# Performance work log

Measured on AMD Instinct MI355X. Metric: run time of the kernel, lower is better.

## Reference

```python
import jax, jax.numpy as jnp
import numpy as np
from jax import lax

B, S, D, V, MAXLEN = 32, 2048, 1024, 32000, 2048
EPS = jnp.finfo(jnp.float32).eps  # torch RMSNorm default eps=None -> finfo eps


def setup_inputs() -> dict:
    key = jax.random.key(0)
    ks = jax.random.split(key, 10)
    w = lambda k, shape: (jax.random.normal(k, shape, jnp.float32) * 0.02)
    return {
        "x": jax.random.randint(ks[0], (B, S), 0, V),
        "emb": w(ks[1], (V, D)),
        "pos": w(ks[2], (MAXLEN, D)),
        "conv_w": w(ks[3], (3, D, D)),            # HIO layout (k, in, out)
        "conv_b": jnp.zeros((D,), jnp.float32),
        "wg1": w(ks[4], (D, D)), "bg1": jnp.zeros((D,), jnp.float32),
        "wmv": w(ks[5], (2 * D, D)), "bmv": jnp.zeros((D,), jnp.float32),
        "wmg": w(ks[6], (2 * D, D)), "bmg": jnp.zeros((D,), jnp.float32),
        "wrg": w(ks[7], (2 * D, D)), "brg": jnp.zeros((D,), jnp.float32),
        "rms_w": jnp.ones((D,), jnp.float32),
        "wp": w(ks[8], (2 * D, V)), "bp": jnp.zeros((V,), jnp.float32),
    }


def _rmsnorm(v, rms_w):
    ms = jnp.mean(v * v, axis=-1, keepdims=True)
    return v * lax.rsqrt(ms + EPS) * rms_w


def reference(x, emb, pos, conv_w, conv_b, wg1, bg1, wmv, bmv, wmg, bmg,
              wrg, brg, rms_w, wp, bp):
    seq_len = x.shape[1]
    h = emb[x] + pos[:seq_len]                     # [B, S, D]
    # Conv1d(D, D, k=3, padding=1) over the sequence axis
    h = lax.conv_general_dilated(h, conv_w, window_strides=(1,),
                                 padding=((1, 1),),
                                 dimension_numbers=("NHC", "HIO", "NHC")) + conv_b
    nodes = h * jax.nn.sigmoid(h @ wg1 + bg1)      # gated nodes [B, S, D]

    curr = nodes[:, :-1, :]                        # nodes_past [B, S-1, D]
    while curr.shape[1] > 1:                       # log2(S) static levels
        if curr.shape[1] % 2 != 0:
            curr = jnp.concatenate([curr, curr[:, -1:, :]], axis=1)
        left = curr[:, 0::2, :]
        right = curr[:, 1::2, :]
        combined = jnp.concatenate([left, right], axis=-1)   # [B, n/2, 2D]
        val = combined @ wmv + bmv
        gate = jax.nn.sigmoid(combined @ wmg + bmg)
        merged = _rmsnorm(val * gate, rms_w)
        res_gate = jax.nn.sigmoid(combined @ wrg + brg)
        residual = (left + right) * 0.5
        curr = res_gate * merged + (1.0 - res_gate) * residual

    root = curr[:, 0, :]                           # [B, D]
    last = nodes[:, -2, :]                         # last of nodes_past
    context = jnp.concatenate([root, last], axis=-1)  # [B, 2D]
    return context @ wp + bp                       # logits [B, V]
```

## Files before the change

kernel.cpp:

```cpp
#include <hip/hip_runtime.h>
#include <stdint.h>

typedef __bf16 bf16_t;
typedef __attribute__((ext_vector_type(8))) __bf16 bf16x8;
typedef __attribute__((ext_vector_type(4))) __bf16 bf16x4;
typedef __attribute__((ext_vector_type(4))) float f32x4;

#define NB 32
#define NS 2048
#define ND 1024
#define NV 32000
#define SP 2050

__device__ __forceinline__ float sigmoid_(float x) { return 1.0f / (1.0f + __expf(-x)); }

__device__ __forceinline__ void gload_lds16(const void* g, void* lds) {
  __builtin_amdgcn_global_load_lds((const __attribute__((address_space(1))) void*)g,
                                   (__attribute__((address_space(3))) void*)lds, 16, 0, 0);
}


__global__ void zero_pad_k(bf16_t* h0p) {
  int i = blockIdx.x;
  int b = i >> 1;
  size_t row = (size_t)b * SP + ((i & 1) ? (SP - 1) : 0);
  bf16x4 z = {};
  *(bf16x4*)(h0p + row * ND + threadIdx.x * 4) = z;
}

__global__ void embed_k(const int* __restrict__ x, const float* __restrict__ emb,
                        const float* __restrict__ pos, bf16_t* __restrict__ h0p) {
  int bs = blockIdx.x;
  int b = bs >> 11, s = bs & (NS - 1);
  int idx = x[bs];
  const float* e = emb + (size_t)idx * ND;
  const float* p = pos + (size_t)s * ND;
  bf16_t* o = h0p + ((size_t)b * SP + s + 1) * ND;
  int d = threadIdx.x * 4;
  f32x4 ev = *(const f32x4*)(e + d);
  f32x4 pv = *(const f32x4*)(p + d);
  bf16x4 ov;
  ov[0] = (bf16_t)(ev[0] + pv[0]);
  ov[1] = (bf16_t)(ev[1] + pv[1]);
  ov[2] = (bf16_t)(ev[2] + pv[2]);
  ov[3] = (bf16_t)(ev[3] + pv[3]);
  *(bf16x4*)(o + d) = ov;
}

__global__ void conv_transpose_k(const float* __restrict__ in, bf16_t* __restrict__ out,
                                 int R, int C) {
  __shared__ float tile[32][33];
  int tc = blockIdx.x * 32, tr = blockIdx.y * 32;
  int tx = threadIdx.x;
  for (int i = threadIdx.y; i < 32; i += 8)
    tile[i][tx] = in[(size_t)(tr + i) * C + tc + tx];
  __syncthreads();
  for (int i = threadIdx.y; i < 32; i += 8)
    out[(size_t)(tc + i) * R + tr + tx] = (bf16_t)tile[tx][i];
}

__global__ void dup_row_k(bf16_t* nodes) {
  int b = blockIdx.x;
  const bf16_t* src = nodes + ((size_t)b * NS + NS - 2) * ND;
  bf16_t* dst = nodes + ((size_t)b * NS + NS - 1) * ND;
  int d = threadIdx.x * 4;
  *(bf16x4*)(dst + d) = *(const bf16x4*)(src + d);
}

__global__ void concat3_k(const float* __restrict__ a, const float* __restrict__ b,
                          const float* __restrict__ c, float* __restrict__ o) {
  int i = blockIdx.x * 256 + threadIdx.x;
  o[i] = i < 1024 ? a[i] : (i < 2048 ? b[i - 1024] : c[i - 2048]);
}

template <int EPI>
__global__ __launch_bounds__(512, 2) void gemm256(
    const bf16_t* __restrict__ A, const bf16_t* __restrict__ Bt,
    const float* __restrict__ bias, const void* aux, void* Cout,
    int M, int N, int K, int lda, int batchShift, int batchPad,
    int GX, int gpx, int nxg, int ych) {
  const int tid = threadIdx.x;
  const int lane = tid & 63;
  const int wave = tid >> 6;
  int n0, m0;
  if (nxg == 0) {
    n0 = (blockIdx.x % GX) * 256;
    m0 = (blockIdx.x / GX) * 256;
  } else {
    const int id = blockIdx.x;
    const int xcd = id & 7;
    const int jb = id >> 3;
    const int xg = xcd % nxg;
    const int ysub = xcd / nxg;
    n0 = (xg * gpx + (jb % gpx)) * 256;
    m0 = (ysub * ych + (jb / gpx)) * 256;
  }
  const int waveM = wave >> 2, waveN = wave & 3;

  __shared__ __align__(16) bf16_t sA[2][256 * 64];
  __shared__ __align__(16) bf16_t sB[2][256 * 64];

  const int srow = tid >> 3;
  const int sj = tid & 7;
  const bf16_t* pA[4];
  const bf16_t* pB[4];
#pragma unroll
  for (int idx = 0; idx < 4; ++idx) {
    int lr = idx * 64 + srow;
    int sc = sj ^ (lr & 7);
    int gm = m0 + lr;
    if (gm > M - 1) gm = M - 1;
    size_t grow = (size_t)gm + (size_t)(((unsigned)gm) >> batchShift) * batchPad;
    pA[idx] = A + grow * (size_t)lda + sc * 8;
    int gn = n0 + lr;
    if (gn > N - 1) gn = N - 1;
    pB[idx] = Bt + (size_t)gn * K + sc * 8;
  }
  const int ldsrow = wave * 8;

  auto stageA4 = [&](int buf) {
#pragma unroll
    for (int idx = 0; idx < 4; ++idx) {
      gload_lds16(pA[idx], &sA[buf][(size_t)(idx * 64 + ldsrow) * 64]);
      pA[idx] += 64;
    }
  };
  auto stageB4 = [&](int buf) {
#pragma unroll
    for (int idx = 0; idx < 4; ++idx) {
      gload_lds16(pB[idx], &sB[buf][(size_t)(idx * 64 + ldsrow) * 64]);
      pB[idx] += 64;
    }
  };

  const int rlane = lane & 15;
  const int klane = lane >> 4;
  int offA[8][2], offB[4][2];
#pragma unroll
  for (int i = 0; i < 8; ++i) {
    int ra = waveM * 128 + i * 16 + rlane;
#pragma unroll
    for (int ks = 0; ks < 2; ++ks)
      offA[i][ks] = ra * 128 + (((ks * 4 + klane) ^ (ra & 7)) << 4);
  }
#pragma unroll
  for (int j = 0; j < 4; ++j) {
    int rb = waveN * 64 + j * 16 + rlane;
#pragma unroll
    for (int ks = 0; ks < 2; ++ks)
      offB[j][ks] = rb * 128 + (((ks * 4 + klane) ^ (rb & 7)) << 4);
  }

  f32x4 acc[8][4] = {};

  const int nt = K >> 6;
  stageA4(0);
  stageB4(0);
  stageB4(1);
  asm volatile("s_waitcnt vmcnt(4)" ::: "memory");
  __builtin_amdgcn_s_barrier();

  for (int tt = 0; tt < nt; tt += 2) {
#pragma unroll
    for (int u = 0; u < 2; ++u) {
      const int t = tt + u;
      bf16x8 bfr[4][2];
#pragma unroll
      for (int j = 0; j < 4; ++j)
#pragma unroll
        for (int ks = 0; ks < 2; ++ks)
          bfr[j][ks] = *(const bf16x8*)((const char*)&sB[u][0] + offB[j][ks]);
      asm volatile("" ::: "memory");
      bf16x8 a0[4][2];
#pragma unroll
      for (int i = 0; i < 4; ++i)
#pragma unroll
        for (int ks = 0; ks < 2; ++ks)
          a0[i][ks] = *(const bf16x8*)((const char*)&sA[u][0] + offA[i][ks]);
      asm volatile("s_waitcnt lgkmcnt(8)" ::: "memory");
      __builtin_amdgcn_s_barrier();
      if (t + 1 < nt) stageA4(u ^ 1);
      if (t + 2 < nt) stageB4(u);
      __builtin_amdgcn_s_setprio(1);
#pragma unroll
      for (int ks = 0; ks < 2; ++ks)
#pragma unroll
        for (int i = 0; i < 4; ++i)
#pragma unroll
          for (int j = 0; j < 4; ++j)
            acc[i][j] = __builtin_amdgcn_mfma_f32_16x16x32_bf16(
                a0[i][ks], bfr[j][ks], acc[i][j], 0, 0, 0);
      __builtin_amdgcn_s_setprio(0);
      bf16x8 a1[4][2];
#pragma unroll
      for (int i = 0; i < 4; ++i)
#pragma unroll
        for (int ks = 0; ks < 2; ++ks)
          a1[i][ks] = *(const bf16x8*)((const char*)&sA[u][0] + offA[4 + i][ks]);
      __builtin_amdgcn_s_setprio(1);
#pragma unroll
      for (int ks = 0; ks < 2; ++ks)
#pragma unroll
        for (int i = 0; i < 4; ++i)
#pragma unroll
          for (int j = 0; j < 4; ++j)
            acc[4 + i][j] = __builtin_amdgcn_mfma_f32_16x16x32_bf16(
                a1[i][ks], bfr[j][ks], acc[4 + i][j], 0, 0, 0);
      __builtin_amdgcn_s_setprio(0);
      if (t + 2 < nt)
        asm volatile("s_waitcnt vmcnt(4)" ::: "memory");
      else
        asm volatile("s_waitcnt vmcnt(0)" ::: "memory");
      __builtin_amdgcn_s_barrier();
    }
  }

  const int colBase = n0 + waveN * 64 + rlane;
#pragma unroll
  for (int i = 0; i < 8; ++i) {
    const int rowBase = m0 + waveM * 128 + i * 16 + klane * 4;
#pragma unroll
    for (int j = 0; j < 4; ++j) {
      const int col = colBase + j * 16;
      const float bv = bias[col];
#pragma unroll
      for (int r = 0; r < 4; ++r) {
        const int row = rowBase + r;
        if (row >= M) continue;
        float v = acc[i][j][r] + bv;
        size_t o = (size_t)row * N + col;
        if constexpr (EPI == 0) {
          ((bf16_t*)Cout)[o] = (bf16_t)v;
        } else if constexpr (EPI == 1) {
          float hh = (float)((const bf16_t*)aux)[o];
          ((bf16_t*)Cout)[o] = (bf16_t)(hh * sigmoid_(v));
        } else {
          ((bf16_t*)Cout)[o] = (bf16_t)(col < 1024 ? v : sigmoid_(v));
        }
      }
    }
  }
}

template <bool ATOMIC>
__global__ __launch_bounds__(256, 2) void gemm128s(
    const bf16_t* __restrict__ A, const bf16_t* __restrict__ Bt,
    const float* __restrict__ bias, float* __restrict__ Cout,
    int M, int kLen, int nxy) {
  const int tid = threadIdx.x;
  const int lane = tid & 63;
  const int wave = tid >> 6;
  const int id = blockIdx.x;
  const int sk = id / nxy;
  const int rb2 = id % nxy;
  const int n0 = (rb2 % 24) * 128;
  const int m0 = (rb2 / 24) * 128;
  const int kOff = sk * kLen;

  const int waveM = wave >> 1, waveN = wave & 1;

  __shared__ __align__(16) bf16_t sA[2][128 * 64];
  __shared__ __align__(16) bf16_t sB[2][128 * 64];

  f32x4 acc[4][4] = {};

  const int srow = wave * 8 + (lane >> 3);
  const int sj = lane & 7;

  auto stage = [&](int buf, int kk0) {
#pragma unroll
    for (int j = 0; j < 4; ++j) {
      int rowT = j * 32 + srow;
      int k8 = sj ^ (rowT & 7);
      int gm = m0 + rowT;
      if (gm > M - 1) gm = M - 1;
      gload_lds16(A + (size_t)gm * 2048 + (kk0 + k8 * 8), &sA[buf][(j * 256 + wave * 64) * 8]);
      int gn = n0 + rowT;
      gload_lds16(Bt + (size_t)gn * 2048 + (kk0 + k8 * 8), &sB[buf][(j * 256 + wave * 64) * 8]);
    }
  };

  stage(0, kOff);
  __syncthreads();

  const int nt = kLen >> 6;
  int cur = 0;
  const int ar = waveM * 64 + (lane & 15);
  const int br = waveN * 64 + (lane & 15);
  const int kb0 = lane >> 4;

  for (int t = 0; t < nt; ++t) {
    if (t + 1 < nt) stage(cur ^ 1, kOff + (t + 1) * 64);

    const bf16_t* sa = sA[cur];
    const bf16_t* sb = sB[cur];
    bf16x8 af[2][4], bfr[2][4];
#pragma unroll
    for (int ks = 0; ks < 2; ++ks) {
      int kb = kb0 + ks * 4;
#pragma unroll
      for (int i = 0; i < 4; ++i) {
        int ra = ar + i * 16;
        af[ks][i] = *(const bf16x8*)&sa[ra * 64 + ((kb ^ (ra & 7)) * 8)];
        int rbq = br + i * 16;
        bfr[ks][i] = *(const bf16x8*)&sb[rbq * 64 + ((kb ^ (rbq & 7)) * 8)];
      }
    }
#pragma unroll
    for (int ks = 0; ks < 2; ++ks)
#pragma unroll
      for (int i = 0; i < 4; ++i)
#pragma unroll
        for (int j = 0; j < 4; ++j)
          acc[i][j] = __builtin_amdgcn_mfma_f32_16x16x32_bf16(af[ks][i], bfr[ks][j], acc[i][j], 0, 0, 0);
    __syncthreads();
    cur ^= 1;
  }

  const int colBase = n0 + waveN * 64 + (lane & 15);
#pragma unroll
  for (int i = 0; i < 4; ++i) {
    const int rowBase = m0 + waveM * 64 + i * 16 + (lane >> 4) * 4;
#pragma unroll
    for (int jj = 0; jj < 4; ++jj) {
      const int col = colBase + jj * 16;
      const float bv = (!ATOMIC || kOff == 0) ? bias[col] : 0.0f;
#pragma unroll
      for (int r = 0; r < 4; ++r) {
        const int row = rowBase + r;
        if (row >= M) continue;
        float v = acc[i][jj][r] + bv;
        size_t o = (size_t)row * 3072 + col;
        if constexpr (ATOMIC)
          atomicAdd(&Cout[o], v);
        else
          Cout[o] = v;
      }
    }
  }
}

__global__ __launch_bounds__(256) void tree_combine_k(
    const bf16_t* __restrict__ fb, const bf16_t* __restrict__ cur,
    const float* __restrict__ rms_w, bf16_t* __restrict__ outb) {
  const int m = blockIdx.x;
  const int t = threadIdx.x;
  const int d = t * 4;
  const bf16_t* row = fb + (size_t)m * 3072;
  bf16x4 vb = *(const bf16x4*)(row + d);
  bf16x4 gb = *(const bf16x4*)(row + 1024 + d);
  bf16x4 rb = *(const bf16x4*)(row + 2048 + d);
  f32x4 vg;
#pragma unroll
  for (int k = 0; k < 4; ++k) vg[k] = (float)vb[k] * (float)gb[k];
  float ss = vg[0] * vg[0] + vg[1] * vg[1] + vg[2] * vg[2] + vg[3] * vg[3];
#pragma unroll
  for (int o = 32; o > 0; o >>= 1) ss += __shfl_xor(ss, o);
  __shared__ float red[4];
  if ((t & 63) == 0) red[t >> 6] = ss;
  __syncthreads();
  float ms = (red[0] + red[1] + red[2] + red[3]) * (1.0f / ND);
  float scale = rsqrtf(ms + 1.1920929e-07f);
  f32x4 w = *(const f32x4*)(rms_w + d);
  const bf16_t* c0 = cur + (size_t)m * 2048;
  bf16x4 lv = *(const bf16x4*)(c0 + d);
  bf16x4 rv = *(const bf16x4*)(c0 + ND + d);
  bf16x4 o4;
#pragma unroll
  for (int k = 0; k < 4; ++k) {
    float merged = vg[k] * scale * w[k];
    float resid = 0.5f * ((float)lv[k] + (float)rv[k]);
    float g = (float)rb[k];
    o4[k] = (bf16_t)(g * merged + (1.0f - g) * resid);
  }
  *(bf16x4*)(outb + (size_t)m * ND + d) = o4;
}

__global__ __launch_bounds__(256) void tree_combine32_k(
    const float* __restrict__ fb, const bf16_t* __restrict__ cur,
    const float* __restrict__ rms_w, bf16_t* __restrict__ outb) {
  const int m = blockIdx.x;
  const int t = threadIdx.x;
  const int d = t * 4;
  const float* row = fb + (size_t)m * 3072;
  f32x4 v = *(const f32x4*)(row + d);
  f32x4 gl = *(const f32x4*)(row + 1024 + d);
  f32x4 rl = *(const f32x4*)(row + 2048 + d);
  f32x4 vg;
#pragma unroll
  for (int k = 0; k < 4; ++k) vg[k] = v[k] * sigmoid_(gl[k]);
  float ss = vg[0] * vg[0] + vg[1] * vg[1] + vg[2] * vg[2] + vg[3] * vg[3];
#pragma unroll
  for (int o = 32; o > 0; o >>= 1) ss += __shfl_xor(ss, o);
  __shared__ float red[4];
  if ((t & 63) == 0) red[t >> 6] = ss;
  __syncthreads();
  float ms = (red[0] + red[1] + red[2] + red[3]) * (1.0f / ND);
  float scale = rsqrtf(ms + 1.1920929e-07f);
  f32x4 w = *(const f32x4*)(rms_w + d);
  const bf16_t* c0 = cur + (size_t)m * 2048;
  bf16x4 lv = *(const bf16x4*)(c0 + d);
  bf16x4 rv = *(const bf16x4*)(c0 + ND + d);
  bf16x4 o4;
#pragma unroll
  for (int k = 0; k < 4; ++k) {
    float merged = vg[k] * scale * w[k];
    float resid = 0.5f * ((float)lv[k] + (float)rv[k]);
    float g = sigmoid_(rl[k]);
    o4[k] = (bf16_t)(g * merged + (1.0f - g) * resid);
  }
  *(bf16x4*)(outb + (size_t)m * ND + d) = o4;
}

__global__ void build_ctx_k(const bf16_t* __restrict__ root, const bf16_t* __restrict__ nodes,
                            bf16_t* __restrict__ ctxb) {
  int b = blockIdx.x, t = threadIdx.x;
  const bf16_t* r = root + (size_t)b * ND;
  const bf16_t* l = nodes + ((size_t)b * NS + NS - 2) * ND;
  int d = t * 4;
  *(bf16x4*)(ctxb + (size_t)b * 2048 + d) = *(const bf16x4*)(r + d);
  *(bf16x4*)(ctxb + (size_t)b * 2048 + ND + d) = *(const bf16x4*)(l + d);
}

__global__ void init_out_k(const float* __restrict__ bp, float* __restrict__ out) {
  int i = blockIdx.x * 256 + threadIdx.x;
  int b = i / NV;
  out[i] = bp[i - b * NV];
}

__global__ __launch_bounds__(256) void proj_gemm_k(
    const bf16_t* __restrict__ ctxb, const bf16_t* __restrict__ wpT,
    float* __restrict__ out) {
  const int lane = threadIdx.x & 63;
  const int wave = threadIdx.x >> 6;
  const int n0 = blockIdx.x * 256 + wave * 64;
  const int kbase = blockIdx.y * 512;
  const int rl = lane & 15, kl = lane >> 4;
  f32x4 acc[2][4] = {};
#pragma unroll 4
  for (int kt = 0; kt < 16; ++kt) {
    const int k0 = kbase + kt * 32 + kl * 8;
    bf16x8 af[2], bfr[4];
#pragma unroll
    for (int i = 0; i < 2; ++i)
      af[i] = *(const bf16x8*)&ctxb[(size_t)(i * 16 + rl) * 2048 + k0];
#pragma unroll
    for (int j = 0; j < 4; ++j)
      bfr[j] = *(const bf16x8*)&wpT[(size_t)(n0 + j * 16 + rl) * 2048 + k0];
#pragma unroll
    for (int i = 0; i < 2; ++i)
#pragma unroll
      for (int j = 0; j < 4; ++j)
        acc[i][j] = __builtin_amdgcn_mfma_f32_16x16x32_bf16(af[i], bfr[j], acc[i][j], 0, 0, 0);
  }
#pragma unroll
  for (int i = 0; i < 2; ++i)
#pragma unroll
    for (int j = 0; j < 4; ++j)
#pragma unroll
      for (int r = 0; r < 4; ++r) {
        int b = i * 16 + kl * 4 + r;
        int v = n0 + j * 16 + rl;
        atomicAdd(&out[(size_t)b * NV + v], acc[i][j][r]);
      }
}

extern "C" void kernel_launch(void* const* d_in, const int* in_sizes, int n_in,
                              void* d_out, int out_size, void* d_ws, size_t ws_size,
                              hipStream_t stream) {
  const int* x = (const int*)d_in[0];
  const float* emb = (const float*)d_in[1];
  const float* pos = (const float*)d_in[2];
  const float* conv_w = (const float*)d_in[3];
  const float* conv_b = (const float*)d_in[4];
  const float* wg1 = (const float*)d_in[5];
  const float* bg1 = (const float*)d_in[6];
  const float* wmv = (const float*)d_in[7];
  const float* bmv = (const float*)d_in[8];
  const float* wmg = (const float*)d_in[9];
  const float* bmg = (const float*)d_in[10];
  const float* wrg = (const float*)d_in[11];
  const float* brg = (const float*)d_in[12];
  const float* rms_w = (const float*)d_in[13];
  const float* wp = (const float*)d_in[14];
  const float* bp = (const float*)d_in[15];
  float* out = (float*)d_out;

  char* ws = (char*)d_ws;
  size_t off = 0;
  auto alloc = [&](size_t bytes) -> void* {
    void* p = ws + off;
    off += (bytes + 255) & ~(size_t)255;
    return p;
  };
  bf16_t* h0p = (bf16_t*)alloc((size_t)NB * SP * ND * 2);
  bf16_t* h = (bf16_t*)alloc((size_t)NB * NS * ND * 2);
  bf16_t* nodes = (bf16_t*)alloc((size_t)NB * NS * ND * 2);
  bf16_t* tb0 = (bf16_t*)alloc((size_t)NB * 1024 * ND * 2);
  bf16_t* tb1 = (bf16_t*)alloc((size_t)NB * 1024 * ND * 2);
  bf16_t* convT = (bf16_t*)alloc((size_t)ND * 3072 * 2);
  bf16_t* wg1T = (bf16_t*)alloc((size_t)ND * 1024 * 2);
  bf16_t* wAllT = (bf16_t*)alloc((size_t)3072 * 2048 * 2);
  float* bAll = (float*)alloc((size_t)3072 * 4);
  bf16_t* ctxb = (bf16_t*)alloc((size_t)NB * 2048 * 2);
  if (off > ws_size) return;
  bf16_t* fbuf = (bf16_t*)ws;
  float* fbuf32 = (float*)ws;
  bf16_t* wpT = (bf16_t*)ws;

  dim3 t256(256), tb32(32, 8);

  conv_transpose_k<<<dim3(ND / 32, 3072 / 32), tb32, 0, stream>>>(conv_w, convT, 3072, ND);
  conv_transpose_k<<<dim3(ND / 32, ND / 32), tb32, 0, stream>>>(wg1, wg1T, ND, ND);
  conv_transpose_k<<<dim3(ND / 32, 2048 / 32), tb32, 0, stream>>>(wmv, wAllT, 2048, ND);
  conv_transpose_k<<<dim3(ND / 32, 2048 / 32), tb32, 0, stream>>>(wmg, wAllT + (size_t)1024 * 2048, 2048, ND);
  conv_transpose_k<<<dim3(ND / 32, 2048 / 32), tb32, 0, stream>>>(wrg, wAllT + (size_t)2048 * 2048, 2048, ND);
  concat3_k<<<12, t256, 0, stream>>>(bmv, bmg, brg, bAll);

  zero_pad_k<<<64, t256, 0, stream>>>(h0p);
  embed_k<<<NB * NS, t256, 0, stream>>>(x, emb, pos, h0p);

  gemm256<0><<<1024, 512, 0, stream>>>(h0p, convT, conv_b, nullptr, h,
                                       NB * NS, ND, 3072, ND, 11, 2, 4, 1, 4, 128);
  gemm256<1><<<1024, 512, 0, stream>>>(h, wg1T, bg1, h, nodes,
                                       NB * NS, ND, ND, ND, 0, 0, 4, 1, 4, 128);
  dup_row_k<<<NB, t256, 0, stream>>>(nodes);

  const bf16_t* cur = nodes;
  bf16_t* bufs[2] = {tb0, tb1};
  int pp = 0;
  for (int L = NS; L > 1; L >>= 1) {
    int M = NB * (L / 2);
    if (M >= 16384) {
      int GY = M / 256;
      gemm256<3><<<12 * GY, 512, 0, stream>>>(cur, wAllT, bAll, nullptr, fbuf,
                                              M, 3072, 2048, 2048, 0, 0, 12, 3, 4, GY / 2);
      tree_combine_k<<<M, t256, 0, stream>>>(fbuf, cur, rms_w, bufs[pp]);
    } else {
      int GY = (M + 127) / 128;
      int nxy = 24 * GY;
      int SK = 1;
      while (nxy * SK < 768 && SK < 16) SK <<= 1;
      if (SK > 1) {
        hipMemsetAsync(fbuf32, 0, (size_t)M * 3072 * 4, stream);
        gemm128s<true><<<nxy * SK, t256, 0, stream>>>(cur, wAllT, bAll, fbuf32,
                                                      M, 2048 / SK, nxy);
      } else {
        gemm128s<false><<<nxy, t256, 0, stream>>>(cur, wAllT, bAll, fbuf32, M, 2048, nxy);
      }
      tree_combine32_k<<<M, t256, 0, stream>>>(fbuf32, cur, rms_w, bufs[pp]);
    }
    cur = bufs[pp];
    pp ^= 1;
  }

  build_ctx_k<<<NB, t256, 0, stream>>>(cur, nodes, ctxb);
  conv_transpose_k<<<dim3(NV / 32, 2048 / 32), tb32, 0, stream>>>(wp, wpT, 2048, NV);
  init_out_k<<<NB * NV / 256, t256, 0, stream>>>(bp, out);
  proj_gemm_k<<<dim3(NV / 256, 4), t256, 0, stream>>>(ctxb, wpT, out);
}
```

Baseline: 2.315 ms.

## Split GEMM K-step into four phases interleaving half-tile loads with MFMA

Restructures the main GEMM inner loop from two big compute phases into four, each loading two A fragments, issuing half of the next A or B tile's global-to-LDS copies, then running 16 MFMAs. The aim is to spread memory issue across the compute so loads and MFMAs overlap more finely, in the style of a ping-pong schedule. It adds more barriers per K-step and a full lgkmcnt(0) wait per phase, which could add synchronisation stalls.

```diff
diff --git a/kernel.cpp b/kernel.cpp
--- a/kernel.cpp
+++ b/kernel.cpp
@@ -118,16 +118,18 @@
   }
   const int ldsrow = wave * 8;
 
-  auto stageA4 = [&](int buf) {
-#pragma unroll
-    for (int idx = 0; idx < 4; ++idx) {
+  auto stageAhalf = [&](int buf, int h) {
+#pragma unroll
+    for (int r = 0; r < 2; ++r) {
+      int idx = h * 2 + r;
       gload_lds16(pA[idx], &sA[buf][(size_t)(idx * 64 + ldsrow) * 64]);
       pA[idx] += 64;
     }
   };
-  auto stageB4 = [&](int buf) {
-#pragma unroll
-    for (int idx = 0; idx < 4; ++idx) {
+  auto stageBhalf = [&](int buf, int h) {
+#pragma unroll
+    for (int r = 0; r < 2; ++r) {
+      int idx = h * 2 + r;
       gload_lds16(pB[idx], &sB[buf][(size_t)(idx * 64 + ldsrow) * 64]);
       pB[idx] += 64;
     }
@@ -154,9 +156,9 @@
   f32x4 acc[8][4] = {};
 
   const int nt = K >> 6;
-  stageA4(0);
-  stageB4(0);
-  stageB4(1);
+  stageAhalf(0, 0); stageAhalf(0, 1);
+  stageBhalf(0, 0); stageBhalf(0, 1);
+  stageBhalf(1, 0); stageBhalf(1, 1);
   asm volatile("s_waitcnt vmcnt(4)" ::: "memory");
   __builtin_amdgcn_s_barrier();
 
@@ -164,54 +166,57 @@
 #pragma unroll
     for (int u = 0; u < 2; ++u) {
       const int t = tt + u;
+      const char* sa = (const char*)&sA[u][0];
+      const char* sb = (const char*)&sB[u][0];
       bf16x8 bfr[4][2];
 #pragma unroll
-      for (int j = 0; j < 4; ++j)
+      for (int p = 0; p < 4; ++p) {
+        if (p == 0) {
+#pragma unroll
+          for (int j = 0; j < 4; ++j)
+#pragma unroll
+            for (int ks = 0; ks < 2; ++ks)
+              bfr[j][ks] = *(const bf16x8*)(sb + offB[j][ks]);
+          asm volatile("" ::: "memory");
+        }
+        bf16x8 av[2][2];
+#pragma unroll
+        for (int i = 0; i < 2; ++i)
+#pragma unroll
+          for (int ks = 0; ks < 2; ++ks)
+            av[i][ks] = *(const bf16x8*)(sa + offA[p * 2 + i][ks]);
+        if (p == 0) {
+          if (t + 1 < nt) stageAhalf(u ^ 1, 0);
+        } else if (p == 1) {
+          if (t + 1 < nt) stageAhalf(u ^ 1, 1);
+        } else if (p == 2) {
+          if (t + 2 < nt) stageBhalf(u, 0);
+        } else {
+          if (t + 2 < nt) stageBhalf(u, 1);
+        }
+        if (p == 0) asm volatile("s_waitcnt lgkmcnt(8)" ::: "memory");
+        __builtin_amdgcn_s_barrier();
+        asm volatile("s_waitcnt lgkmcnt(0)" ::: "memory");
+        __builtin_amdgcn_s_setprio(1);
 #pragma unroll
         for (int ks = 0; ks < 2; ++ks)
-          bfr[j][ks] = *(const bf16x8*)((const char*)&sB[u][0] + offB[j][ks]);
-      asm volatile("" ::: "memory");
-      bf16x8 a0[4][2];
-#pragma unroll
-      for (int i = 0; i < 4; ++i)
-#pragma unroll
-        for (int ks = 0; ks < 2; ++ks)
-          a0[i][ks] = *(const bf16x8*)((const char*)&sA[u][0] + offA[i][ks]);
-      asm volatile("s_waitcnt lgkmcnt(8)" ::: "memory");
-      __builtin_amdgcn_s_barrier();
-      if (t + 1 < nt) stageA4(u ^ 1);
-      if (t + 2 < nt) stageB4(u);
-      __builtin_amdgcn_s_setprio(1);
-#pragma unroll
-      for (int ks = 0; ks < 2; ++ks)
-#pragma unroll
-        for (int i = 0; i < 4; ++i)
-#pragma unroll
-          for (int j = 0; j < 4; ++j)
-            acc[i][j] = __builtin_amdgcn_mfma_f32_16x16x32_bf16(
-                a0[i][ks], bfr[j][ks], acc[i][j], 0, 0, 0);
-      __builtin_amdgcn_s_setprio(0);
-      bf16x8 a1[4][2];
-#pragma unroll
-      for (int i = 0; i < 4; ++i)
-#pragma unroll
-        for (int ks = 0; ks < 2; ++ks)
-          a1[i][ks] = *(const bf16x8*)((const char*)&sA[u][0] + offA[4 + i][ks]);
-      __builtin_amdgcn_s_setprio(1);
-#pragma unroll
-      for (int ks = 0; ks < 2; ++ks)
-#pragma unroll
-        for (int i = 0; i < 4; ++i)
-#pragma unroll
-          for (int j = 0; j < 4; ++j)
-            acc[4 + i][j] = __builtin_amdgcn_mfma_f32_16x16x32_bf16(
-                a1[i][ks], bfr[j][ks], acc[4 + i][j], 0, 0, 0);
-      __builtin_amdgcn_s_setprio(0);
-      if (t + 2 < nt)
-        asm volatile("s_waitcnt vmcnt(4)" ::: "memory");
-      else
-        asm volatile("s_waitcnt vmcnt(0)" ::: "memory");
-      __builtin_amdgcn_s_barrier();
+#pragma unroll
+          for (int i = 0; i < 2; ++i)
+#pragma unroll
+            for (int j = 0; j < 4; ++j)
+              acc[p * 2 + i][j] = __builtin_amdgcn_mfma_f32_16x16x32_bf16(
+                  av[i][ks], bfr[j][ks], acc[p * 2 + i][j], 0, 0, 0);
+        __builtin_amdgcn_s_setprio(0);
+        if (p < 3) {
+          __builtin_amdgcn_s_barrier();
+        } else {
+          if (t + 2 < nt)
+            asm volatile("s_waitcnt vmcnt(4)" ::: "memory");
+          else
+            asm volatile("s_waitcnt vmcnt(0)" ::: "memory");
+          __builtin_amdgcn_s_barrier();
+        }
+      }
     }
   }
 
```

After: 2.332 ms, median of 2. No clear change (+0.7%).
